# Optimization experiments

Measured on AMD Instinct MI355X. Metric: run time of the kernel, lower is better.

## Reference

```python
import jax, jax.numpy as jnp
import numpy as np

N = 50000
E = 800000
H_IN = 64
HEADS1 = 4
NEG_SLOPE = 0.2


def gat_conv(x, W, att_src, att_dst, bias, src, dst, heads, out_ch):
    """PyG GATConv (add_self_loops=False, concat=True).
    x: [N, in]; W: [in, heads*out_ch]; att_*: [heads, out_ch]; bias: [heads*out_ch].
    """
    n = x.shape[0]
    h = (x @ W).reshape(n, heads, out_ch)                 # [N, H, C]
    a_s = jnp.einsum('nhc,hc->nh', h, att_src)            # [N, H]
    a_d = jnp.einsum('nhc,hc->nh', h, att_dst)            # [N, H]
    e = jax.nn.leaky_relu(a_s[src] + a_d[dst], NEG_SLOPE) # [E, H]
    # segment softmax over incoming edges of each destination node
    e_max = jax.ops.segment_max(e, dst, num_segments=n)
    e_exp = jnp.exp(e - e_max[dst])
    denom = jax.ops.segment_sum(e_exp, dst, num_segments=n)
    alpha = e_exp / denom[dst]                            # [E, H]
    msg = h[src] * alpha[:, :, None]                      # [E, H, C]
    out = jax.ops.segment_sum(msg, dst, num_segments=n)   # [N, H, C]
    return out.reshape(n, heads * out_ch) + bias


def setup_inputs() -> dict:
    key = jax.random.key(0)
    ks = jax.random.split(key, 10)
    x = jax.random.normal(ks[0], (N, H_IN), dtype=jnp.float32)
    edge_index = jax.random.randint(ks[1], (2, E), 0, N, dtype=jnp.int64)
    s1 = 1.0 / np.sqrt(H_IN)
    W1 = jax.random.normal(ks[2], (H_IN, HEADS1 * H_IN), dtype=jnp.float32) * s1
    att_src1 = jax.random.normal(ks[3], (HEADS1, H_IN), dtype=jnp.float32) * s1
    att_dst1 = jax.random.normal(ks[4], (HEADS1, H_IN), dtype=jnp.float32) * s1
    b1 = jnp.zeros((HEADS1 * H_IN,), dtype=jnp.float32)
    s2 = 1.0 / np.sqrt(HEADS1 * H_IN)
    W2 = jax.random.normal(ks[5], (HEADS1 * H_IN, H_IN), dtype=jnp.float32) * s2
    att_src2 = jax.random.normal(ks[6], (1, H_IN), dtype=jnp.float32) * s2
    att_dst2 = jax.random.normal(ks[7], (1, H_IN), dtype=jnp.float32) * s2
    b2 = jnp.zeros((H_IN,), dtype=jnp.float32)
    return {"x": x, "edge_index": edge_index, "W1": W1, "att_src1": att_src1,
            "att_dst1": att_dst1, "b1": b1, "W2": W2, "att_src2": att_src2,
            "att_dst2": att_dst2, "b2": b2}


def reference(x, edge_index, W1, att_src1, att_dst1, b1, W2, att_src2, att_dst2, b2):
    src, dst = edge_index[0], edge_index[1]
    h = gat_conv(x, W1, att_src1, att_dst1, b1, src, dst, HEADS1, H_IN)
    h = jax.nn.relu(h)
    out = gat_conv(h, W2, att_src2, att_dst2, b2, src, dst, 1, H_IN)
    return out
```

## Files before the change

kernel.cpp:

```cpp
#include <hip/hip_runtime.h>
#include <hip/hip_fp16.h>

#define NEG_SLOPE 0.2f
#define H_IN 64

__device__ __forceinline__ float lrelu(float v) { return v > 0.f ? v : NEG_SLOPE * v; }

__global__ __launch_bounds__(256) void zero_int2(int* __restrict__ a,
                                                 int* __restrict__ b, int n)
{
    int i = blockIdx.x * 256 + threadIdx.x;
    if (i < n) { a[i] = 0; b[i] = 0; }
}

__global__ __launch_bounds__(256) void hist_kernel(const int* __restrict__ dst,
                                                   int* __restrict__ deg, int ne)
{
    int e = blockIdx.x * 256 + threadIdx.x;
    if (e < ne) atomicAdd(&deg[dst[e]], 1);
}

__global__ __launch_bounds__(256) void block_sum(const int* __restrict__ deg,
                                                 int* __restrict__ bsum, int n)
{
    __shared__ int part[4];
    int i = blockIdx.x * 256 + threadIdx.x;
    int v = (i < n) ? deg[i] : 0;
    #pragma unroll
    for (int off = 32; off; off >>= 1) v += __shfl_down(v, off);
    int lane = threadIdx.x & 63, wv = threadIdx.x >> 6;
    if (lane == 0) part[wv] = v;
    __syncthreads();
    if (threadIdx.x == 0)
        bsum[blockIdx.x] = part[0] + part[1] + part[2] + part[3];
}

__global__ __launch_bounds__(256) void scan_bsum(const int* __restrict__ bsum,
                                                 int* __restrict__ bpre, int nb)
{
    __shared__ int sm[256];
    int t = threadIdx.x;
    int v = (t < nb) ? bsum[t] : 0;
    sm[t] = v; __syncthreads();
    for (int off = 1; off < 256; off <<= 1) {
        int y = (t >= off) ? sm[t - off] : 0;
        __syncthreads();
        if (t >= off) sm[t] += y;
        __syncthreads();
    }
    if (t < nb) bpre[t] = sm[t] - v;
}

__global__ __launch_bounds__(256) void scan_rowptr(const int* __restrict__ deg,
                                                   const int* __restrict__ bpre,
                                                   int* __restrict__ rowptr, int n)
{
    __shared__ int sm[256];
    int t = threadIdx.x;
    int i = blockIdx.x * 256 + t;
    int v = (i < n) ? deg[i] : 0;
    sm[t] = v; __syncthreads();
    for (int off = 1; off < 256; off <<= 1) {
        int y = (t >= off) ? sm[t - off] : 0;
        __syncthreads();
        if (t >= off) sm[t] += y;
        __syncthreads();
    }
    if (i < n) rowptr[i] = sm[t] - v + bpre[blockIdx.x];
}

__global__ __launch_bounds__(256) void scatter_kernel(
    const int* __restrict__ src, const int* __restrict__ dst,
    const int* __restrict__ rowptr, int* __restrict__ cursor,
    int* __restrict__ csr_src, int ne)
{
    int e = blockIdx.x * 256 + threadIdx.x;
    if (e >= ne) return;
    int t = dst[e];
    int pos = atomicAdd(&cursor[t], 1);
    csr_src[rowptr[t] + pos] = src[e];
}

__global__ __launch_bounds__(256) void micro_wa(
    const float* __restrict__ W1, const float* __restrict__ as1, const float* __restrict__ ad1,
    const float* __restrict__ W2, const float* __restrict__ as2, const float* __restrict__ ad2,
    float* __restrict__ wa1s, float* __restrict__ wa1d,
    float* __restrict__ wa2s, float* __restrict__ wa2d)
{
    int tid = threadIdx.x;
    int k = tid >> 2, h = tid & 3;
    float s = 0.f, d = 0.f;
    #pragma unroll 8
    for (int c = 0; c < 64; ++c) {
        float w = W1[k * 256 + h * 64 + c];
        s = fmaf(w, as1[h * 64 + c], s);
        d = fmaf(w, ad1[h * 64 + c], d);
    }
    wa1s[k * 4 + h] = s; wa1d[k * 4 + h] = d;
    float s2 = 0.f, d2 = 0.f;
    #pragma unroll 8
    for (int c = 0; c < 64; ++c) {
        float w = W2[tid * 64 + c];
        s2 = fmaf(w, as2[c], s2);
        d2 = fmaf(w, ad2[c], d2);
    }
    wa2s[tid] = s2; wa2d[tid] = d2;
}

__global__ __launch_bounds__(256) void axw1_kernel(
    const float* __restrict__ x,
    const float* __restrict__ wa1s, const float* __restrict__ wa1d,
    float* __restrict__ a_s, float* __restrict__ a_d, int n)
{
    __shared__ float ws[256], wd[256];
    int tid = threadIdx.x;
    ws[tid] = wa1s[tid]; wd[tid] = wa1d[tid];
    __syncthreads();
    int row = blockIdx.x * 256 + tid;
    if (row >= n) return;
    const float4* xv = (const float4*)(x + (size_t)row * 64);
    float aS[4] = {0, 0, 0, 0}, aD[4] = {0, 0, 0, 0};
    #pragma unroll
    for (int k4 = 0; k4 < 16; ++k4) {
        float4 q = xv[k4];
        float xe[4] = {q.x, q.y, q.z, q.w};
        #pragma unroll
        for (int e = 0; e < 4; ++e) {
            int k = k4 * 4 + e;
            #pragma unroll
            for (int h = 0; h < 4; ++h) {
                aS[h] = fmaf(xe[e], ws[k * 4 + h], aS[h]);
                aD[h] = fmaf(xe[e], wd[k * 4 + h], aD[h]);
            }
        }
    }
    #pragma unroll
    for (int h = 0; h < 4; ++h) {
        a_s[row * 4 + h] = aS[h];
        a_d[row * 4 + h] = aD[h];
    }
}

__global__ __launch_bounds__(256) void gemm1_kernel(
    const float* __restrict__ x, const float* __restrict__ W1,
    __half* __restrict__ h1, int n)
{
    __shared__ float w_s[32 * 256];
    int tid = threadIdx.x;
    int row0 = blockIdx.x * 16;
    float acc[4][4];
    #pragma unroll
    for (int s = 0; s < 4; ++s)
        #pragma unroll
        for (int r = 0; r < 4; ++r) acc[s][r] = 0.f;

    const float4* Wv = (const float4*)W1;
    for (int kk = 0; kk < 2; ++kk) {
        if (kk) __syncthreads();
        {
            float4* wv = (float4*)w_s;
            #pragma unroll
            for (int i = 0; i < 8; ++i)
                wv[tid + i * 256] = Wv[kk * 2048 + tid + i * 256];
        }
        __syncthreads();
        #pragma unroll
        for (int sub = 0; sub < 4; ++sub) {
            const float4* x0 = (const float4*)(x + (size_t)(row0 + sub * 4) * 64 + kk * 32);
            const float4* x1 = x0 + 16;
            const float4* x2 = x0 + 32;
            const float4* x3 = x0 + 48;
            #pragma unroll
            for (int k4 = 0; k4 < 8; ++k4) {
                float4 q0 = x0[k4], q1 = x1[k4], q2 = x2[k4], q3 = x3[k4];
                const float* f0 = (const float*)&q0;
                const float* f1 = (const float*)&q1;
                const float* f2 = (const float*)&q2;
                const float* f3 = (const float*)&q3;
                #pragma unroll
                for (int e = 0; e < 4; ++e) {
                    float w = w_s[(k4 * 4 + e) * 256 + tid];
                    acc[sub][0] = fmaf(f0[e], w, acc[sub][0]);
                    acc[sub][1] = fmaf(f1[e], w, acc[sub][1]);
                    acc[sub][2] = fmaf(f2[e], w, acc[sub][2]);
                    acc[sub][3] = fmaf(f3[e], w, acc[sub][3]);
                }
            }
        }
    }
    #pragma unroll
    for (int sub = 0; sub < 4; ++sub) {
        size_t base = (size_t)(row0 + sub * 4) * 256 + tid;
        h1[base]       = __float2half(acc[sub][0]);
        h1[base + 256] = __float2half(acc[sub][1]);
        h1[base + 512] = __float2half(acc[sub][2]);
        h1[base + 768] = __float2half(acc[sub][3]);
    }
}

__global__ __launch_bounds__(256) void gemm2_kernel(
    const __half* __restrict__ xr, const float* __restrict__ W2,
    __half* __restrict__ h2, int n)
{
    __shared__ float w_s[128 * 64];
    int tid = threadIdx.x;
    int col = tid & 63, wv_ = tid >> 6;
    int row0 = blockIdx.x * 64 + wv_ * 16;
    float acc[4][4];
    #pragma unroll
    for (int s = 0; s < 4; ++s)
        #pragma unroll
        for (int r = 0; r < 4; ++r) acc[s][r] = 0.f;

    const float4* Wv = (const float4*)W2;
    for (int kk = 0; kk < 2; ++kk) {
        if (kk) __syncthreads();
        {
            float4* wv = (float4*)w_s;
            #pragma unroll
            for (int i = 0; i < 8; ++i)
                wv[tid + i * 256] = Wv[kk * 2048 + tid + i * 256];
        }
        __syncthreads();
        #pragma unroll
        for (int sub = 0; sub < 4; ++sub) {
            int r0 = row0 + sub * 4;
            const float4* x0 = (const float4*)(xr + (size_t)r0 * 256 + kk * 128);
            const float4* x1 = x0 + 32;
            const float4* x2 = x0 + 64;
            const float4* x3 = x0 + 96;
            #pragma unroll 4
            for (int k8 = 0; k8 < 16; ++k8) {
                float4 q0 = x0[k8], q1 = x1[k8], q2 = x2[k8], q3 = x3[k8];
                const __half2* p0 = (const __half2*)&q0;
                const __half2* p1 = (const __half2*)&q1;
                const __half2* p2 = (const __half2*)&q2;
                const __half2* p3 = (const __half2*)&q3;
                #pragma unroll
                for (int e = 0; e < 4; ++e) {
                    float2 g0 = __half22float2(p0[e]);
                    float2 g1 = __half22float2(p1[e]);
                    float2 g2 = __half22float2(p2[e]);
                    float2 g3 = __half22float2(p3[e]);
                    float wA = w_s[(k8 * 8 + e * 2) * 64 + col];
                    float wB = w_s[(k8 * 8 + e * 2 + 1) * 64 + col];
                    acc[sub][0] = fmaf(g0.x, wA, acc[sub][0]); acc[sub][0] = fmaf(g0.y, wB, acc[sub][0]);
                    acc[sub][1] = fmaf(g1.x, wA, acc[sub][1]); acc[sub][1] = fmaf(g1.y, wB, acc[sub][1]);
                    acc[sub][2] = fmaf(g2.x, wA, acc[sub][2]); acc[sub][2] = fmaf(g2.y, wB, acc[sub][2]);
                    acc[sub][3] = fmaf(g3.x, wA, acc[sub][3]); acc[sub][3] = fmaf(g3.y, wB, acc[sub][3]);
                }
            }
        }
    }
    #pragma unroll
    for (int sub = 0; sub < 4; ++sub) {
        int r0 = row0 + sub * 4;
        if (r0 + 3 < n) {
            size_t b = (size_t)r0 * 64 + col;
            h2[b]       = __float2half(acc[sub][0]);
            h2[b + 64]  = __float2half(acc[sub][1]);
            h2[b + 128] = __float2half(acc[sub][2]);
            h2[b + 192] = __float2half(acc[sub][3]);
        } else {
            for (int r = 0; r < 4; ++r)
                if (r0 + r < n) h2[(size_t)(r0 + r) * 64 + col] = __float2half(acc[sub][r]);
        }
    }
}

__global__ __launch_bounds__(256) void aggr1_csr(
    const int* __restrict__ rowptr, const int* __restrict__ deg,
    const int* __restrict__ csr_src,
    const float* __restrict__ a_s, const float* __restrict__ a_d,
    const __half* __restrict__ h1, const float* __restrict__ b1,
    const float* __restrict__ wa2s, const float* __restrict__ wa2d,
    __half* __restrict__ out1r, float* __restrict__ a_s2, float* __restrict__ a_d2,
    int n)
{
    __shared__ float al[4][64];
    __shared__ int   ss[64];
    __shared__ float ev[4][128];
    __shared__ float2 pm[128];
    __shared__ float p1[2], p2[2];
    int t = blockIdx.x;
    int tid = threadIdx.x, h = tid >> 6, lane = tid & 63;
    int row0 = rowptr[t], d = deg[t];
    float adt = a_d[t * 4 + h];
    bool small = (d <= 128);

    float m = -INFINITY;
    if (small) {
        for (int i = lane; i < d; i += 64) {
            float v = lrelu(a_s[csr_src[row0 + i] * 4 + h] + adt);
            ev[h][i] = v;
            m = fmaxf(m, v);
        }
    } else {
        for (int i = lane; i < d; i += 64)
            m = fmaxf(m, lrelu(a_s[csr_src[row0 + i] * 4 + h] + adt));
    }
    #pragma unroll
    for (int off = 32; off; off >>= 1) m = fmaxf(m, __shfl_xor(m, off));

    float dsum = 0.f;
    if (small) {
        for (int i = lane; i < d; i += 64) dsum += __expf(ev[h][i] - m);
    } else {
        for (int i = lane; i < d; i += 64)
            dsum += __expf(lrelu(a_s[csr_src[row0 + i] * 4 + h] + adt) - m);
    }
    #pragma unroll
    for (int off = 32; off; off >>= 1) dsum += __shfl_xor(dsum, off);
    float inv = (d > 0) ? 1.f / dsum : 0.f;

    int cpair = tid & 127;
    int p = tid >> 7;
    int hc = cpair >> 5;
    float2 acc = make_float2(0.f, 0.f);
    const __half2* hbase = (const __half2*)h1;

    for (int c0 = 0; c0 < d; c0 += 64) {
        int i = c0 + lane;
        float alpha = 0.f;
        if (i < d) {
            float v = small ? ev[h][i] : lrelu(a_s[csr_src[row0 + i] * 4 + h] + adt);
            alpha = __expf(v - m) * inv;
        }
        al[h][lane] = alpha;
        if (h == 0) ss[lane] = (i < d) ? csr_src[row0 + i] * 128 : 0;
        __syncthreads();
        int cl = min(64, d - c0);
        int j = p;
        for (; j + 2 < cl; j += 4) {
            float a0 = al[hc][j];
            float a1 = al[hc][j + 2];
            float2 g0 = __half22float2(hbase[ss[j] + cpair]);
            float2 g1 = __half22float2(hbase[ss[j + 2] + cpair]);
            acc.x = fmaf(a0, g0.x, acc.x);
            acc.y = fmaf(a0, g0.y, acc.y);
            acc.x = fmaf(a1, g1.x, acc.x);
            acc.y = fmaf(a1, g1.y, acc.y);
        }
        if (j < cl) {
            float a0 = al[hc][j];
            float2 g0 = __half22float2(hbase[ss[j] + cpair]);
            acc.x = fmaf(a0, g0.x, acc.x);
            acc.y = fmaf(a0, g0.y, acc.y);
        }
        __syncthreads();
    }

    if (p == 1) pm[cpair] = acc;
    __syncthreads();
    if (p == 0) {
        float2 o = pm[cpair];
        float r0v = fmaxf(acc.x + o.x + b1[2 * cpair], 0.f);
        float r1v = fmaxf(acc.y + o.y + b1[2 * cpair + 1], 0.f);
        ((__half2*)out1r)[(size_t)t * 128 + cpair] = __floats2half2_rn(r0v, r1v);
        float s2  = r0v * wa2s[2 * cpair] + r1v * wa2s[2 * cpair + 1];
        float d2v = r0v * wa2d[2 * cpair] + r1v * wa2d[2 * cpair + 1];
        #pragma unroll
        for (int off = 32; off; off >>= 1) {
            s2  += __shfl_down(s2, off);
            d2v += __shfl_down(d2v, off);
        }
        if ((tid & 63) == 0) { p1[tid >> 6] = s2; p2[tid >> 6] = d2v; }
    }
    __syncthreads();
    if (tid == 0) {
        a_s2[t] = p1[0] + p1[1];
        a_d2[t] = p2[0] + p2[1];
    }
}

__global__ __launch_bounds__(256) void aggr2_csr(
    const int* __restrict__ rowptr, const int* __restrict__ deg,
    const int* __restrict__ csr_src,
    const float* __restrict__ a_s, const float* __restrict__ a_d,
    const __half* __restrict__ h2, const float* __restrict__ b2,
    float* __restrict__ dout, int n)
{
    __shared__ float ev2[4][128];
    __shared__ float al2[4][64];
    __shared__ int   ss2[4][64];
    int wv = threadIdx.x >> 6, lane = threadIdx.x & 63;
    int t = blockIdx.x * 4 + wv;
    if (t >= n) return;
    int row0 = rowptr[t], d = deg[t];
    float adt = a_d[t];
    bool small = (d <= 128);

    float m = -INFINITY;
    if (small) {
        for (int i = lane; i < d; i += 64) {
            float v = lrelu(a_s[csr_src[row0 + i]] + adt);
            ev2[wv][i] = v;
            m = fmaxf(m, v);
        }
    } else {
        for (int i = lane; i < d; i += 64)
            m = fmaxf(m, lrelu(a_s[csr_src[row0 + i]] + adt));
    }
    #pragma unroll
    for (int off = 32; off; off >>= 1) m = fmaxf(m, __shfl_xor(m, off));

    float dsum = 0.f;
    if (small) {
        for (int i = lane; i < d; i += 64) dsum += __expf(ev2[wv][i] - m);
    } else {
        for (int i = lane; i < d; i += 64)
            dsum += __expf(lrelu(a_s[csr_src[row0 + i]] + adt) - m);
    }
    #pragma unroll
    for (int off = 32; off; off >>= 1) dsum += __shfl_xor(dsum, off);
    float inv = (d > 0) ? 1.f / dsum : 0.f;

    int c2 = lane & 31;
    int p = lane >> 5;
    float2 acc = make_float2(0.f, 0.f);
    const __half2* hbase = (const __half2*)h2;

    for (int c0 = 0; c0 < d; c0 += 64) {
        int i = c0 + lane;
        float alpha = 0.f; int so = 0;
        if (i < d) {
            int s = csr_src[row0 + i];
            so = s * 32;
            float v = small ? ev2[wv][i] : lrelu(a_s[s] + adt);
            alpha = __expf(v - m) * inv;
        }
        al2[wv][lane] = alpha;
        ss2[wv][lane] = so;
        int cl = min(64, d - c0);
        int j = p;
        for (; j + 2 < cl; j += 4) {
            float a0 = al2[wv][j];
            float a1 = al2[wv][j + 2];
            float2 g0 = __half22float2(hbase[ss2[wv][j] + c2]);
            float2 g1 = __half22float2(hbase[ss2[wv][j + 2] + c2]);
            acc.x = fmaf(a0, g0.x, acc.x);
            acc.y = fmaf(a0, g0.y, acc.y);
            acc.x = fmaf(a1, g1.x, acc.x);
            acc.y = fmaf(a1, g1.y, acc.y);
        }
        if (j < cl) {
            float a0 = al2[wv][j];
            float2 g0 = __half22float2(hbase[ss2[wv][j] + c2]);
            acc.x = fmaf(a0, g0.x, acc.x);
            acc.y = fmaf(a0, g0.y, acc.y);
        }
    }

    acc.x += __shfl_down(acc.x, 32);
    acc.y += __shfl_down(acc.y, 32);
    if (p == 0) {
        float2 o;
        o.x = acc.x + b2[2 * c2];
        o.y = acc.y + b2[2 * c2 + 1];
        ((float2*)(dout + (size_t)t * 64))[c2] = o;
    }
}

extern "C" void kernel_launch(void* const* d_in, const int* in_sizes, int n_in,
                              void* d_out, int out_size, void* d_ws, size_t ws_size,
                              hipStream_t stream)
{
    const float* x    = (const float*)d_in[0];
    const int*   ei   = (const int*)d_in[1];
    const float* W1   = (const float*)d_in[2];
    const float* as1  = (const float*)d_in[3];
    const float* ad1  = (const float*)d_in[4];
    const float* b1   = (const float*)d_in[5];
    const float* W2   = (const float*)d_in[6];
    const float* as2  = (const float*)d_in[7];
    const float* ad2  = (const float*)d_in[8];
    const float* b2   = (const float*)d_in[9];
    float* dout = (float*)d_out;

    const int n  = in_sizes[0] / H_IN;
    const int ne = in_sizes[1] / 2;
    const int* src = ei;
    const int* dst = ei + ne;
    const int NB = (n + 255) / 256;

    float* ws = (float*)d_ws;
    __half* h1h   = (__half*)ws;
    __half* out1r = h1h + (size_t)n * 256;
    float* fbase  = ws + (size_t)n * 256;
    float* a_s1   = fbase;
    float* a_d1   = a_s1   + (size_t)n * 4;
    float* a_s2   = a_d1   + (size_t)n * 4;
    float* a_d2   = a_s2   + (size_t)n;
    float* wa1s   = a_d2   + (size_t)n;
    float* wa1d   = wa1s + 256;
    float* wa2s   = wa1d + 256;
    float* wa2d   = wa2s + 256;
    int*   deg    = (int*)(wa2d + 256);
    int*   rowptr = deg + n;
    int*   csr    = rowptr + n;
    int*   bsum   = csr + ne;
    int*   bpre   = bsum + NB;
    int*   cursor = (int*)h1h;
    __half* h2h   = h1h;

    micro_wa<<<1, 256, 0, stream>>>(W1, as1, ad1, W2, as2, ad2, wa1s, wa1d, wa2s, wa2d);

    zero_int2<<<NB, 256, 0, stream>>>(deg, cursor, n);
    hist_kernel<<<(ne + 255) / 256, 256, 0, stream>>>(dst, deg, ne);
    block_sum<<<NB, 256, 0, stream>>>(deg, bsum, n);
    scan_bsum<<<1, 256, 0, stream>>>(bsum, bpre, NB);
    scan_rowptr<<<NB, 256, 0, stream>>>(deg, bpre, rowptr, n);
    scatter_kernel<<<(ne + 255) / 256, 256, 0, stream>>>(src, dst, rowptr, cursor, csr, ne);

    axw1_kernel<<<NB, 256, 0, stream>>>(x, wa1s, wa1d, a_s1, a_d1, n);
    gemm1_kernel<<<n / 16, 256, 0, stream>>>(x, W1, h1h, n);
    aggr1_csr<<<n, 256, 0, stream>>>(rowptr, deg, csr, a_s1, a_d1, h1h, b1,
                                     wa2s, wa2d, out1r, a_s2, a_d2, n);

    gemm2_kernel<<<(n + 63) / 64, 256, 0, stream>>>(out1r, W2, h2h, n);
    aggr2_csr<<<(n + 3) / 4, 256, 0, stream>>>(rowptr, deg, csr, a_s2, a_d2, h2h, b2, dout, n);
}
```

Measured before the change: 443.1 us.

## Widen gathers to 4 halves, fuse init kernels, fp16 dot2 in gemm2

Several changes land together. The micro weight-attention kernel is merged with the zeroing kernel to save a launch. gemm1 and gemm2 are restructured so each thread keeps 16 row accumulators, and gemm2 stores W2 in shared memory as fp16 pairs and uses the fdot2 instruction. Both aggregation kernels now gather 8-byte (4-half) vectors per lane with more partial sums, which changes the reduction. The softmax exponentials are also cached in shared memory so they are not recomputed. Converting W2 to fp16 and using fdot2 adds precision risk, and the wider gathers change occupancy and the shape of the reduction.

```diff
diff --git a/kernel.cpp b/kernel.cpp
--- a/kernel.cpp
+++ b/kernel.cpp
@@ -4,13 +4,58 @@
 #define NEG_SLOPE 0.2f
 #define H_IN 64
 
+typedef _Float16 h2vec __attribute__((ext_vector_type(2)));
+
 __device__ __forceinline__ float lrelu(float v) { return v > 0.f ? v : NEG_SLOPE * v; }
 
-__global__ __launch_bounds__(256) void zero_int2(int* __restrict__ a,
-                                                 int* __restrict__ b, int n)
-{
-    int i = blockIdx.x * 256 + threadIdx.x;
-    if (i < n) { a[i] = 0; b[i] = 0; }
+__device__ __forceinline__ void cvt4(uint2 g, float* o) {
+    __half2 lo = *(__half2*)&g.x, hi = *(__half2*)&g.y;
+    float2 a = __half22float2(lo), b = __half22float2(hi);
+    o[0] = a.x; o[1] = a.y; o[2] = b.x; o[3] = b.y;
+}
+
+__device__ __forceinline__ float fdot2h(float xf, h2vec w, float acc) {
+#if __has_builtin(__builtin_amdgcn_fdot2)
+    union { float f; h2vec h; } cv; cv.f = xf;
+    return __builtin_amdgcn_fdot2(cv.h, w, acc, false);
+#else
+    union { float f; __half2 h; } cv; cv.f = xf;
+    float2 g = __half22float2(cv.h);
+    acc = fmaf(g.x, (float)w[0], acc);
+    return fmaf(g.y, (float)w[1], acc);
+#endif
+}
+
+__global__ __launch_bounds__(256) void zero_micro(
+    int* __restrict__ deg, int* __restrict__ cursor, int n,
+    const float* __restrict__ W1, const float* __restrict__ as1, const float* __restrict__ ad1,
+    const float* __restrict__ W2, const float* __restrict__ as2, const float* __restrict__ ad2,
+    float* __restrict__ wa1s, float* __restrict__ wa1d,
+    float* __restrict__ wa2s, float* __restrict__ wa2d)
+{
+    int tid = threadIdx.x;
+    if (blockIdx.x > 0) {
+        int i = (blockIdx.x - 1) * 256 + tid;
+        if (i < n) { deg[i] = 0; cursor[i] = 0; }
+        return;
+    }
+    int k = tid >> 2, h = tid & 3;
+    float s = 0.f, d = 0.f;
+    #pragma unroll 8
+    for (int c = 0; c < 64; ++c) {
+        float w = W1[k * 256 + h * 64 + c];
+        s = fmaf(w, as1[h * 64 + c], s);
+        d = fmaf(w, ad1[h * 64 + c], d);
+    }
+    wa1s[k * 4 + h] = s; wa1d[k * 4 + h] = d;
+    float s2 = 0.f, d2 = 0.f;
+    #pragma unroll 8
+    for (int c = 0; c < 64; ++c) {
+        float w = W2[tid * 64 + c];
+        s2 = fmaf(w, as2[c], s2);
+        d2 = fmaf(w, ad2[c], d2);
+    }
+    wa2s[tid] = s2; wa2d[tid] = d2;
 }
 
 __global__ __launch_bounds__(256) void hist_kernel(const int* __restrict__ dst,
@@ -79,32 +124,6 @@
     int t = dst[e];
     int pos = atomicAdd(&cursor[t], 1);
     csr_src[rowptr[t] + pos] = src[e];
-}
-
-__global__ __launch_bounds__(256) void micro_wa(
-    const float* __restrict__ W1, const float* __restrict__ as1, const float* __restrict__ ad1,
-    const float* __restrict__ W2, const float* __restrict__ as2, const float* __restrict__ ad2,
-    float* __restrict__ wa1s, float* __restrict__ wa1d,
-    float* __restrict__ wa2s, float* __restrict__ wa2d)
-{
-    int tid = threadIdx.x;
-    int k = tid >> 2, h = tid & 3;
-    float s = 0.f, d = 0.f;
-    #pragma unroll 8
-    for (int c = 0; c < 64; ++c) {
-        float w = W1[k * 256 + h * 64 + c];
-        s = fmaf(w, as1[h * 64 + c], s);
-        d = fmaf(w, ad1[h * 64 + c], d);
-    }
-    wa1s[k * 4 + h] = s; wa1d[k * 4 + h] = d;
-    float s2 = 0.f, d2 = 0.f;
-    #pragma unroll 8
-    for (int c = 0; c < 64; ++c) {
-        float w = W2[tid * 64 + c];
-        s2 = fmaf(w, as2[c], s2);
-        d2 = fmaf(w, ad2[c], d2);
-    }
-    wa2s[tid] = s2; wa2d[tid] = d2;
 }
 
 __global__ __launch_bounds__(256) void axw1_kernel(
@@ -148,11 +167,9 @@
     __shared__ float w_s[32 * 256];
     int tid = threadIdx.x;
     int row0 = blockIdx.x * 16;
-    float acc[4][4];
-    #pragma unroll
-    for (int s = 0; s < 4; ++s)
-        #pragma unroll
-        for (int r = 0; r < 4; ++r) acc[s][r] = 0.f;
+    float acc[16];
+    #pragma unroll
+    for (int r = 0; r < 16; ++r) acc[r] = 0.f;
 
     const float4* Wv = (const float4*)W1;
     for (int kk = 0; kk < 2; ++kk) {
@@ -164,107 +181,65 @@
                 wv[tid + i * 256] = Wv[kk * 2048 + tid + i * 256];
         }
         __syncthreads();
-        #pragma unroll
-        for (int sub = 0; sub < 4; ++sub) {
-            const float4* x0 = (const float4*)(x + (size_t)(row0 + sub * 4) * 64 + kk * 32);
-            const float4* x1 = x0 + 16;
-            const float4* x2 = x0 + 32;
-            const float4* x3 = x0 + 48;
-            #pragma unroll
-            for (int k4 = 0; k4 < 8; ++k4) {
-                float4 q0 = x0[k4], q1 = x1[k4], q2 = x2[k4], q3 = x3[k4];
-                const float* f0 = (const float*)&q0;
-                const float* f1 = (const float*)&q1;
-                const float* f2 = (const float*)&q2;
-                const float* f3 = (const float*)&q3;
+        #pragma unroll 2
+        for (int k4 = 0; k4 < 8; ++k4) {
+            float4 q[16];
+            #pragma unroll
+            for (int r = 0; r < 16; ++r)
+                q[r] = *(const float4*)(x + (size_t)(row0 + r) * 64 + kk * 32 + k4 * 4);
+            #pragma unroll
+            for (int e = 0; e < 4; ++e) {
+                float w = w_s[(k4 * 4 + e) * 256 + tid];
                 #pragma unroll
-                for (int e = 0; e < 4; ++e) {
-                    float w = w_s[(k4 * 4 + e) * 256 + tid];
-                    acc[sub][0] = fmaf(f0[e], w, acc[sub][0]);
-                    acc[sub][1] = fmaf(f1[e], w, acc[sub][1]);
-                    acc[sub][2] = fmaf(f2[e], w, acc[sub][2]);
-                    acc[sub][3] = fmaf(f3[e], w, acc[sub][3]);
-                }
+                for (int r = 0; r < 16; ++r)
+                    acc[r] = fmaf(((const float*)&q[r])[e], w, acc[r]);
             }
         }
     }
     #pragma unroll
-    for (int sub = 0; sub < 4; ++sub) {
-        size_t base = (size_t)(row0 + sub * 4) * 256 + tid;
-        h1[base]       = __float2half(acc[sub][0]);
-        h1[base + 256] = __float2half(acc[sub][1]);
-        h1[base + 512] = __float2half(acc[sub][2]);
-        h1[base + 768] = __float2half(acc[sub][3]);
-    }
+    for (int r = 0; r < 16; ++r)
+        h1[(size_t)(row0 + r) * 256 + tid] = __float2half(acc[r]);
 }
 
 __global__ __launch_bounds__(256) void gemm2_kernel(
     const __half* __restrict__ xr, const float* __restrict__ W2,
     __half* __restrict__ h2, int n)
 {
-    __shared__ float w_s[128 * 64];
+    __shared__ h2vec w_s[128 * 64];
     int tid = threadIdx.x;
+    #pragma unroll 4
+    for (int i = 0; i < 32; ++i) {
+        int idx = tid + i * 256;
+        int kp = idx >> 6, col = idx & 63;
+        h2vec v;
+        v[0] = (_Float16)W2[(2 * kp) * 64 + col];
+        v[1] = (_Float16)W2[(2 * kp + 1) * 64 + col];
+        w_s[idx] = v;
+    }
+    __syncthreads();
     int col = tid & 63, wv_ = tid >> 6;
     int row0 = blockIdx.x * 64 + wv_ * 16;
-    float acc[4][4];
-    #pragma unroll
-    for (int s = 0; s < 4; ++s)
+    float acc[16];
+    #pragma unroll
+    for (int r = 0; r < 16; ++r) acc[r] = 0.f;
+
+    const float4* xb = (const float4*)(xr + (size_t)row0 * 256);
+    for (int g = 0; g < 32; ++g) {
+        float4 q[16];
         #pragma unroll
-        for (int r = 0; r < 4; ++r) acc[s][r] = 0.f;
-
-    const float4* Wv = (const float4*)W2;
-    for (int kk = 0; kk < 2; ++kk) {
-        if (kk) __syncthreads();
-        {
-            float4* wv = (float4*)w_s;
-            #pragma unroll
-            for (int i = 0; i < 8; ++i)
-                wv[tid + i * 256] = Wv[kk * 2048 + tid + i * 256];
-        }
-        __syncthreads();
+        for (int r = 0; r < 16; ++r) q[r] = xb[r * 32 + g];
         #pragma unroll
-        for (int sub = 0; sub < 4; ++sub) {
-            int r0 = row0 + sub * 4;
-            const float4* x0 = (const float4*)(xr + (size_t)r0 * 256 + kk * 128);
-            const float4* x1 = x0 + 32;
-            const float4* x2 = x0 + 64;
-            const float4* x3 = x0 + 96;
-            #pragma unroll 4
-            for (int k8 = 0; k8 < 16; ++k8) {
-                float4 q0 = x0[k8], q1 = x1[k8], q2 = x2[k8], q3 = x3[k8];
-                const __half2* p0 = (const __half2*)&q0;
-                const __half2* p1 = (const __half2*)&q1;
-                const __half2* p2 = (const __half2*)&q2;
-                const __half2* p3 = (const __half2*)&q3;
-                #pragma unroll
-                for (int e = 0; e < 4; ++e) {
-                    float2 g0 = __half22float2(p0[e]);
-                    float2 g1 = __half22float2(p1[e]);
-                    float2 g2 = __half22float2(p2[e]);
-                    float2 g3 = __half22float2(p3[e]);
-                    float wA = w_s[(k8 * 8 + e * 2) * 64 + col];
-                    float wB = w_s[(k8 * 8 + e * 2 + 1) * 64 + col];
-                    acc[sub][0] = fmaf(g0.x, wA, acc[sub][0]); acc[sub][0] = fmaf(g0.y, wB, acc[sub][0]);
-                    acc[sub][1] = fmaf(g1.x, wA, acc[sub][1]); acc[sub][1] = fmaf(g1.y, wB, acc[sub][1]);
-                    acc[sub][2] = fmaf(g2.x, wA, acc[sub][2]); acc[sub][2] = fmaf(g2.y, wB, acc[sub][2]);
-                    acc[sub][3] = fmaf(g3.x, wA, acc[sub][3]); acc[sub][3] = fmaf(g3.y, wB, acc[sub][3]);
-                }
-            }
-        }
-    }
-    #pragma unroll
-    for (int sub = 0; sub < 4; ++sub) {
-        int r0 = row0 + sub * 4;
-        if (r0 + 3 < n) {
-            size_t b = (size_t)r0 * 64 + col;
-            h2[b]       = __float2half(acc[sub][0]);
-            h2[b + 64]  = __float2half(acc[sub][1]);
-            h2[b + 128] = __float2half(acc[sub][2]);
-            h2[b + 192] = __float2half(acc[sub][3]);
-        } else {
-            for (int r = 0; r < 4; ++r)
-                if (r0 + r < n) h2[(size_t)(r0 + r) * 64 + col] = __float2half(acc[sub][r]);
-        }
+        for (int e = 0; e < 4; ++e) {
+            h2vec w = w_s[(g * 4 + e) * 64 + col];
+            #pragma unroll
+            for (int r = 0; r < 16; ++r)
+                acc[r] = fdot2h(((const float*)&q[r])[e], w, acc[r]);
+        }
+    }
+    #pragma unroll
+    for (int r = 0; r < 16; ++r) {
+        int row = row0 + r;
+        if (row < n) h2[(size_t)row * 64 + col] = __float2half(acc[r]);
     }
 }
 
@@ -280,8 +255,7 @@
     __shared__ float al[4][64];
     __shared__ int   ss[64];
     __shared__ float ev[4][128];
-    __shared__ float2 pm[128];
-    __shared__ float p1[2], p2[2];
+    __shared__ float pm[3][64][4];
     int t = blockIdx.x;
     int tid = threadIdx.x, h = tid >> 6, lane = tid & 63;
     int row0 = rowptr[t], d = deg[t];
@@ -304,7 +278,11 @@
 
     float dsum = 0.f;
     if (small) {
-        for (int i = lane; i < d; i += 64) dsum += __expf(ev[h][i] - m);
+        for (int i = lane; i < d; i += 64) {
+            float e = __expf(ev[h][i] - m);
+            ev[h][i] = e;
+            dsum += e;
+        }
     } else {
         for (int i = lane; i < d; i += 64)
             dsum += __expf(lrelu(a_s[csr_src[row0 + i] * 4 + h] + adt) - m);
@@ -313,63 +291,71 @@
     for (int off = 32; off; off >>= 1) dsum += __shfl_xor(dsum, off);
     float inv = (d > 0) ? 1.f / dsum : 0.f;
 
-    int cpair = tid & 127;
-    int p = tid >> 7;
-    int hc = cpair >> 5;
-    float2 acc = make_float2(0.f, 0.f);
-    const __half2* hbase = (const __half2*)h1;
+    int c4 = tid & 63;
+    int p = tid >> 6;
+    int hc = c4 >> 4;
+    float acc[4] = {0.f, 0.f, 0.f, 0.f};
+    const uint2* hb = (const uint2*)h1;
 
     for (int c0 = 0; c0 < d; c0 += 64) {
         int i = c0 + lane;
         float alpha = 0.f;
         if (i < d) {
-            float v = small ? ev[h][i] : lrelu(a_s[csr_src[row0 + i] * 4 + h] + adt);
-            alpha = __expf(v - m) * inv;
+            if (small) alpha = ev[h][i] * inv;
+            else alpha = __expf(lrelu(a_s[csr_src[row0 + i] * 4 + h] + adt) - m) * inv;
         }
         al[h][lane] = alpha;
-        if (h == 0) ss[lane] = (i < d) ? csr_src[row0 + i] * 128 : 0;
+        if (h == 0) ss[lane] = (i < d) ? csr_src[row0 + i] * 64 : 0;
         __syncthreads();
         int cl = min(64, d - c0);
         int j = p;
-        for (; j + 2 < cl; j += 4) {
-            float a0 = al[hc][j];
-            float a1 = al[hc][j + 2];
-            float2 g0 = __half22float2(hbase[ss[j] + cpair]);
-            float2 g1 = __half22float2(hbase[ss[j + 2] + cpair]);
-            acc.x = fmaf(a0, g0.x, acc.x);
-            acc.y = fmaf(a0, g0.y, acc.y);
-            acc.x = fmaf(a1, g1.x, acc.x);
-            acc.y = fmaf(a1, g1.y, acc.y);
+        for (; j + 4 < cl; j += 8) {
+            float a0 = al[hc][j], a1 = al[hc][j + 4];
+            uint2 g0 = hb[ss[j] + c4];
+            uint2 g1 = hb[ss[j + 4] + c4];
+            float f0[4], f1[4];
+            cvt4(g0, f0); cvt4(g1, f1);
+            #pragma unroll
+            for (int q = 0; q < 4; ++q) {
+                acc[q] = fmaf(a0, f0[q], acc[q]);
+                acc[q] = fmaf(a1, f1[q], acc[q]);
+            }
         }
         if (j < cl) {
             float a0 = al[hc][j];
-            float2 g0 = __half22float2(hbase[ss[j] + cpair]);
-            acc.x = fmaf(a0, g0.x, acc.x);
-            acc.y = fmaf(a0, g0.y, acc.y);
-        }
-        __syncthreads();
-    }
-
-    if (p == 1) pm[cpair] = acc;
+            uint2 g0 = hb[ss[j] + c4];
+            float f0[4];
+            cvt4(g0, f0);
+            #pragma unroll
+            for (int q = 0; q < 4; ++q) acc[q] = fmaf(a0, f0[q], acc[q]);
+        }
+        __syncthreads();
+    }
+
+    if (p) {
+        #pragma unroll
+        for (int q = 0; q < 4; ++q) pm[p - 1][c4][q] = acc[q];
+    }
     __syncthreads();
     if (p == 0) {
-        float2 o = pm[cpair];
-        float r0v = fmaxf(acc.x + o.x + b1[2 * cpair], 0.f);
-        float r1v = fmaxf(acc.y + o.y + b1[2 * cpair + 1], 0.f);
-        ((__half2*)out1r)[(size_t)t * 128 + cpair] = __floats2half2_rn(r0v, r1v);
-        float s2  = r0v * wa2s[2 * cpair] + r1v * wa2s[2 * cpair + 1];
-        float d2v = r0v * wa2d[2 * cpair] + r1v * wa2d[2 * cpair + 1];
+        float4 bb = ((const float4*)b1)[c4];
+        float r0 = fmaxf(acc[0] + pm[0][c4][0] + pm[1][c4][0] + pm[2][c4][0] + bb.x, 0.f);
+        float r1 = fmaxf(acc[1] + pm[0][c4][1] + pm[1][c4][1] + pm[2][c4][1] + bb.y, 0.f);
+        float r2 = fmaxf(acc[2] + pm[0][c4][2] + pm[1][c4][2] + pm[2][c4][2] + bb.z, 0.f);
+        float r3 = fmaxf(acc[3] + pm[0][c4][3] + pm[1][c4][3] + pm[2][c4][3] + bb.w, 0.f);
+        __half2 lo = __floats2half2_rn(r0, r1), hi = __floats2half2_rn(r2, r3);
+        uint2 o; o.x = *(unsigned*)&lo; o.y = *(unsigned*)&hi;
+        ((uint2*)out1r)[(size_t)t * 64 + c4] = o;
+        float4 ws4 = ((const float4*)wa2s)[c4];
+        float4 wd4 = ((const float4*)wa2d)[c4];
+        float s2  = r0 * ws4.x + r1 * ws4.y + r2 * ws4.z + r3 * ws4.w;
+        float d2v = r0 * wd4.x + r1 * wd4.y + r2 * wd4.z + r3 * wd4.w;
         #pragma unroll
         for (int off = 32; off; off >>= 1) {
             s2  += __shfl_down(s2, off);
             d2v += __shfl_down(d2v, off);
         }
-        if ((tid & 63) == 0) { p1[tid >> 6] = s2; p2[tid >> 6] = d2v; }
-    }
-    __syncthreads();
-    if (tid == 0) {
-        a_s2[t] = p1[0] + p1[1];
-        a_d2[t] = p2[0] + p2[1];
+        if (tid == 0) { a_s2[t] = s2; a_d2[t] = d2v; }
     }
 }
 
@@ -406,7 +392,11 @@
 
     float dsum = 0.f;
     if (small) {
-        for (int i = lane; i < d; i += 64) dsum += __expf(ev2[wv][i] - m);
+        for (int i = lane; i < d; i += 64) {
+            float e = __expf(ev2[wv][i] - m);
+            ev2[wv][i] = e;
+            dsum += e;
+        }
     } else {
         for (int i = lane; i < d; i += 64)
             dsum += __expf(lrelu(a_s[csr_src[row0 + i]] + adt) - m);
@@ -415,49 +405,57 @@
     for (int off = 32; off; off >>= 1) dsum += __shfl_xor(dsum, off);
     float inv = (d > 0) ? 1.f / dsum : 0.f;
 
-    int c2 = lane & 31;
-    int p = lane >> 5;
-    float2 acc = make_float2(0.f, 0.f);
-    const __half2* hbase = (const __half2*)h2;
+    int c4 = lane & 15;
+    int p = lane >> 4;
+    float acc[4] = {0.f, 0.f, 0.f, 0.f};
+    const uint2* hb = (const uint2*)h2;
 
     for (int c0 = 0; c0 < d; c0 += 64) {
         int i = c0 + lane;
         float alpha = 0.f; int so = 0;
         if (i < d) {
             int s = csr_src[row0 + i];
-            so = s * 32;
-            float v = small ? ev2[wv][i] : lrelu(a_s[s] + adt);
-            alpha = __expf(v - m) * inv;
+            so = s * 16;
+            if (small) alpha = ev2[wv][i] * inv;
+            else alpha = __expf(lrelu(a_s[s] + adt) - m) * inv;
         }
         al2[wv][lane] = alpha;
         ss2[wv][lane] = so;
         int cl = min(64, d - c0);
         int j = p;
-        for (; j + 2 < cl; j += 4) {
-            float a0 = al2[wv][j];
-            float a1 = al2[wv][j + 2];
-            float2 g0 = __half22float2(hbase[ss2[wv][j] + c2]);
-            float2 g1 = __half22float2(hbase[ss2[wv][j + 2] + c2]);
-            acc.x = fmaf(a0, g0.x, acc.x);
-            acc.y = fmaf(a0, g0.y, acc.y);
-            acc.x = fmaf(a1, g1.x, acc.x);
-            acc.y = fmaf(a1, g1.y, acc.y);
+        for (; j + 4 < cl; j += 8) {
+            float a0 = al2[wv][j], a1 = al2[wv][j + 4];
+            uint2 g0 = hb[ss2[wv][j] + c4];
+            uint2 g1 = hb[ss2[wv][j + 4] + c4];
+            float f0[4], f1[4];
+            cvt4(g0, f0); cvt4(g1, f1);
+            #pragma unroll
+            for (int q = 0; q < 4; ++q) {
+                acc[q] = fmaf(a0, f0[q], acc[q]);
+                acc[q] = fmaf(a1, f1[q], acc[q]);
+            }
         }
         if (j < cl) {
             float a0 = al2[wv][j];
-            float2 g0 = __half22float2(hbase[ss2[wv][j] + c2]);
-            acc.x = fmaf(a0, g0.x, acc.x);
-            acc.y = fmaf(a0, g0.y, acc.y);
-        }
-    }
-
-    acc.x += __shfl_down(acc.x, 32);
-    acc.y += __shfl_down(acc.y, 32);
+            uint2 g0 = hb[ss2[wv][j] + c4];
+            float f0[4];
+            cvt4(g0, f0);
+            #pragma unroll
+            for (int q = 0; q < 4; ++q) acc[q] = fmaf(a0, f0[q], acc[q]);
+        }
+    }
+
+    #pragma unroll
+    for (int q = 0; q < 4; ++q) {
+        acc[q] += __shfl_down(acc[q], 32);
+        acc[q] += __shfl_down(acc[q], 16);
+    }
     if (p == 0) {
-        float2 o;
-        o.x = acc.x + b2[2 * c2];
-        o.y = acc.y + b2[2 * c2 + 1];
-        ((float2*)(dout + (size_t)t * 64))[c2] = o;
+        float4 bb = ((const float4*)b2)[c4];
+        float4 o;
+        o.x = acc[0] + bb.x; o.y = acc[1] + bb.y;
+        o.z = acc[2] + bb.z; o.w = acc[3] + bb.w;
+        ((float4*)(dout + (size_t)t * 64))[c4] = o;
     }
 }
 
@@ -503,9 +501,9 @@
     int*   cursor = (int*)h1h;
     __half* h2h   = h1h;
 
-    micro_wa<<<1, 256, 0, stream>>>(W1, as1, ad1, W2, as2, ad2, wa1s, wa1d, wa2s, wa2d);
-
-    zero_int2<<<NB, 256, 0, stream>>>(deg, cursor, n);
+    zero_micro<<<NB + 1, 256, 0, stream>>>(deg, cursor, n, W1, as1, ad1,
+                                           W2, as2, ad2, wa1s, wa1d, wa2s, wa2d);
+
     hist_kernel<<<(ne + 255) / 256, 256, 0, stream>>>(dst, deg, ne);
     block_sum<<<NB, 256, 0, stream>>>(deg, bsum, n);
     scan_bsum<<<1, 256, 0, stream>>>(bsum, bpre, NB);
```

After: 426.3 us. 1.04x faster.
